# Optimization experiments

Hardware: AMD Instinct MI355X
Metric: run time of the kernel (lower is better)

Reference implementation:

```python
import jax, jax.numpy as jnp
import numpy as np

N_NODES = 50000
N_EDGES = 800000


def gcn_layer(x, edge_index, W, b):
    # GCNConv with normalize=False: out[i] = sum_{(j->i) in E} (x_j @ W) + b
    src, dst = edge_index[0], edge_index[1]
    h = x @ W                          # [N, F_out] transform first (cheaper)
    msg = h[src]                       # [E, F_out] gather
    agg = jax.ops.segment_sum(msg, dst, num_segments=x.shape[0])  # scatter-sum
    return agg + b


def setup_inputs() -> dict:
    key = jax.random.key(0)
    ks = jax.random.split(key, 6)
    x = jax.random.normal(ks[0], (N_NODES, 128), dtype=jnp.float32)
    edge_index = jax.random.randint(ks[1], (2, N_EDGES), 0, N_NODES, dtype=jnp.int64)
    # Glorot-ish scaling for stability through 3 layers
    W1 = jax.random.normal(ks[2], (128, 256), dtype=jnp.float32) * (1.0 / np.sqrt(128))
    W2 = jax.random.normal(ks[3], (256, 256), dtype=jnp.float32) * (1.0 / np.sqrt(256))
    W3 = jax.random.normal(ks[4], (256, 256), dtype=jnp.float32) * (1.0 / np.sqrt(256))
    b1 = jnp.zeros((256,), jnp.float32)
    b2 = jnp.zeros((256,), jnp.float32)
    b3 = jnp.zeros((256,), jnp.float32)
    return {"x": x, "edge_index": edge_index, "W1": W1, "b1": b1,
            "W2": W2, "b2": b2, "W3": W3, "b3": b3}


def reference(x, edge_index, W1, b1, W2, b2, W3, b3):
    h = jax.nn.relu(gcn_layer(x, edge_index, W1, b1))
    h = jax.nn.relu(gcn_layer(h, edge_index, W2, b2))
    h = jax.nn.relu(gcn_layer(h, edge_index, W3, b3))
    return h
```

## Files before the change

### kernel.cpp

```cpp
#include <hip/hip_runtime.h>
#include <hip/hip_bf16.h>


#define NBIN 98
#define BINSH 9

typedef short bf16x8 __attribute__((ext_vector_type(8)));
typedef float f32x4 __attribute__((ext_vector_type(4)));

__device__ __forceinline__ short f2bf(float f) {
    __hip_bfloat16 b = __float2bfloat16(f);
    return *reinterpret_cast<short*>(&b);
}
__device__ __forceinline__ float bf2f(short s) {
    union { unsigned u; float f; } c;
    c.u = ((unsigned)(unsigned short)s) << 16;
    return c.f;
}

__global__ void prep(const float* __restrict__ W1, const float* __restrict__ W2,
                     const float* __restrict__ W3, const float4* __restrict__ x,
                     short* __restrict__ Wt1, short* __restrict__ Wt2,
                     short* __restrict__ Wt3, short* __restrict__ xb) {
    int idx = blockIdx.x * 256 + threadIdx.x;
    if (idx < 32768) {
        int n = idx >> 7, k = idx & 127;
        Wt1[idx] = f2bf(W1[k * 256 + n]);
    } else if (idx < 98304) {
        int i = idx - 32768, n = i >> 8, k = i & 255;
        Wt2[i] = f2bf(W2[k * 256 + n]);
    } else if (idx < 163840) {
        int i = idx - 98304, n = i >> 8, k = i & 255;
        Wt3[i] = f2bf(W3[k * 256 + n]);
    } else {
        int i = idx - 163840;
        if (i < 1600000) {
            float4 v = x[i];
            short tmp[4] = { f2bf(v.x), f2bf(v.y), f2bf(v.z), f2bf(v.w) };
            *reinterpret_cast<uint2*>(&xb[i * 4]) = *reinterpret_cast<uint2*>(tmp);
        }
    }
}


__global__ void coarse_hist(const int* __restrict__ ei, int* __restrict__ cbin, int E) {
    __shared__ int h[NBIN];
    for (int i = threadIdx.x; i < NBIN; i += 256) h[i] = 0;
    __syncthreads();
    int base = blockIdx.x * 4096;
#pragma unroll
    for (int i = 0; i < 16; ++i) {
        int e = base + i * 256 + threadIdx.x;
        if (e < E) atomicAdd(&h[ei[E + e] >> BINSH], 1);
    }
    __syncthreads();
    for (int i = threadIdx.x; i < NBIN; i += 256)
        if (h[i]) atomicAdd(&cbin[i], h[i]);
}

__global__ void coarse_scan(const int* __restrict__ cbin, int* __restrict__ cstart,
                            int* __restrict__ gcursor, int* __restrict__ off,
                            int E, int N) {
    __shared__ int lds[128];
    int v = (threadIdx.x < NBIN) ? cbin[threadIdx.x] : 0;
    lds[threadIdx.x] = v;
    __syncthreads();
    for (int d = 1; d < 128; d <<= 1) {
        int t = (threadIdx.x >= d) ? lds[threadIdx.x - d] : 0;
        __syncthreads();
        lds[threadIdx.x] += t;
        __syncthreads();
    }
    if (threadIdx.x < NBIN) {
        int ex = lds[threadIdx.x] - v;
        cstart[threadIdx.x] = ex;
        gcursor[threadIdx.x] = ex;
    }
    if (threadIdx.x == 0) { cstart[NBIN] = E; off[N] = E; }
}

__global__ void bin_fill(const int* __restrict__ ei, int* __restrict__ gcursor,
                         unsigned* __restrict__ staging, int E) {
    __shared__ int h[NBIN];
    __shared__ int cur[NBIN];
    for (int i = threadIdx.x; i < NBIN; i += 256) h[i] = 0;
    __syncthreads();
    int base = blockIdx.x * 4096;
    int d_[16], s_[16];
#pragma unroll
    for (int i = 0; i < 16; ++i) {
        int e = base + i * 256 + threadIdx.x;
        if (e < E) {
            s_[i] = ei[e];
            d_[i] = ei[E + e];
            atomicAdd(&h[d_[i] >> BINSH], 1);
        } else d_[i] = -1;
    }
    __syncthreads();
    for (int i = threadIdx.x; i < NBIN; i += 256)
        cur[i] = h[i] ? atomicAdd(&gcursor[i], h[i]) : 0;
    __syncthreads();
#pragma unroll
    for (int i = 0; i < 16; ++i) {
        if (d_[i] >= 0) {
            int p = atomicAdd(&cur[d_[i] >> BINSH], 1);
            staging[p] = ((unsigned)(d_[i] & 511) << 16) | (unsigned)s_[i];
        }
    }
}

__global__ void bin_finalize(const unsigned* __restrict__ staging,
                             const int* __restrict__ cstart,
                             int* __restrict__ off, int* __restrict__ csr, int N) {
    __shared__ int cnt[512];
    __shared__ int psum[256];
    __shared__ int cur[512];
    const int b = blockIdx.x, t = threadIdx.x;
    cnt[t] = 0; cnt[t + 256] = 0;
    __syncthreads();
    const int s = cstart[b], e = cstart[b + 1];
    for (int p = s + t; p < e; p += 256) atomicAdd(&cnt[staging[p] >> 16], 1);
    __syncthreads();
    int c0 = cnt[2 * t], c1 = cnt[2 * t + 1];
    psum[t] = c0 + c1;
    __syncthreads();
    for (int d = 1; d < 256; d <<= 1) {
        int v = (t >= d) ? psum[t - d] : 0;
        __syncthreads();
        psum[t] += v;
        __syncthreads();
    }
    int base = s + (t ? psum[t - 1] : 0);
    int nb0 = b << BINSH;
    cur[2 * t] = base;
    cur[2 * t + 1] = base + c0;
    if (nb0 + 2 * t < N)     off[nb0 + 2 * t]     = base;
    if (nb0 + 2 * t + 1 < N) off[nb0 + 2 * t + 1] = base + c0;
    __syncthreads();
    for (int p = s + t; p < e; p += 256) {
        unsigned v = staging[p];
        int pos = atomicAdd(&cur[v >> 16], 1);
        csr[pos] = (int)(v & 0xFFFFu);
    }
}


template <int VEC>
__global__ void gather_csr_bf16(const short* __restrict__ h, short* __restrict__ agg,
                                const int* __restrict__ off, const int* __restrict__ csr,
                                int N) {
    typedef short svec __attribute__((ext_vector_type(VEC)));
    const int gw = (blockIdx.x * blockDim.x + threadIdx.x) >> 6;
    if (gw >= N) return;
    const int lane = threadIdx.x & 63;
    const int col = lane * VEC;
    const int F = 64 * VEC;
    const int base = off[gw];
    const int d = off[gw + 1] - base;

    float acc[VEC];
#pragma unroll
    for (int q = 0; q < VEC; ++q) acc[q] = 0.0f;

    int j = 0;
    for (; j + 4 <= d; j += 4) {
        int s0 = csr[base + j], s1 = csr[base + j + 1];
        int s2 = csr[base + j + 2], s3 = csr[base + j + 3];
        svec v0 = *reinterpret_cast<const svec*>(h + (size_t)s0 * F + col);
        svec v1 = *reinterpret_cast<const svec*>(h + (size_t)s1 * F + col);
        svec v2 = *reinterpret_cast<const svec*>(h + (size_t)s2 * F + col);
        svec v3 = *reinterpret_cast<const svec*>(h + (size_t)s3 * F + col);
#pragma unroll
        for (int q = 0; q < VEC; ++q)
            acc[q] += (bf2f(v0[q]) + bf2f(v1[q])) + (bf2f(v2[q]) + bf2f(v3[q]));
    }
    for (; j < d; ++j) {
        int s = csr[base + j];
        svec v = *reinterpret_cast<const svec*>(h + (size_t)s * F + col);
#pragma unroll
        for (int q = 0; q < VEC; ++q) acc[q] += bf2f(v[q]);
    }
    svec o;
#pragma unroll
    for (int q = 0; q < VEC; ++q) o[q] = f2bf(acc[q]);
    *reinterpret_cast<svec*>(agg + (size_t)gw * F + col) = o;
}


template <typename OutT>
__launch_bounds__(512)
__global__ void gemm_bias_relu(const short* __restrict__ A, const short* __restrict__ Wt,
                               const float* __restrict__ bias, OutT* __restrict__ out,
                               int M, int K) {
    __shared__ short As[128][72];
    __shared__ short Bs[256][72];

    const int tid = threadIdx.x;
    const int lane = tid & 63, wid = tid >> 6;
    const int wr = wid >> 2, wc = wid & 3;
    const int lr = lane & 15, lg = lane >> 4;
    const int m0 = blockIdx.x * 128;

    f32x4 acc[4][4];
#pragma unroll
    for (int i = 0; i < 4; ++i)
#pragma unroll
        for (int j = 0; j < 4; ++j)
#pragma unroll
            for (int r = 0; r < 4; ++r) acc[i][j][r] = 0.0f;

    const int srA = tid >> 2;
    const int scA = (tid & 3) << 4;
    const int srB = tid >> 1;
    const int scB = (tid & 1) << 5;

    for (int k0 = 0; k0 < K; k0 += 64) {
        __syncthreads();
        {
            int gm = m0 + srA;
            if (gm < M) {
                const uint4* ap = reinterpret_cast<const uint4*>(A + (size_t)gm * K + k0 + scA);
                *reinterpret_cast<uint4*>(&As[srA][scA])     = ap[0];
                *reinterpret_cast<uint4*>(&As[srA][scA + 8]) = ap[1];
            } else {
                uint4 z = {0, 0, 0, 0};
                *reinterpret_cast<uint4*>(&As[srA][scA])     = z;
                *reinterpret_cast<uint4*>(&As[srA][scA + 8]) = z;
            }
            const uint4* bp = reinterpret_cast<const uint4*>(Wt + (size_t)srB * K + k0 + scB);
            *reinterpret_cast<uint4*>(&Bs[srB][scB])      = bp[0];
            *reinterpret_cast<uint4*>(&Bs[srB][scB + 8])  = bp[1];
            *reinterpret_cast<uint4*>(&Bs[srB][scB + 16]) = bp[2];
            *reinterpret_cast<uint4*>(&Bs[srB][scB + 24]) = bp[3];
        }
        __syncthreads();

#pragma unroll
        for (int ksub = 0; ksub < 2; ++ksub) {
            const int kb = ksub * 32 + 4 * lg;
            bf16x8 a[4], b[4];
#pragma unroll
            for (int mi = 0; mi < 4; ++mi) {
                int row = wr * 64 + mi * 16 + lr;
                uint2* pa = reinterpret_cast<uint2*>(&a[mi]);
                pa[0] = *reinterpret_cast<const uint2*>(&As[row][kb]);
                pa[1] = *reinterpret_cast<const uint2*>(&As[row][kb + 16]);
            }
#pragma unroll
            for (int ni = 0; ni < 4; ++ni) {
                int row = wc * 64 + ni * 16 + lr;
                uint2* pb = reinterpret_cast<uint2*>(&b[ni]);
                pb[0] = *reinterpret_cast<const uint2*>(&Bs[row][kb]);
                pb[1] = *reinterpret_cast<const uint2*>(&Bs[row][kb + 16]);
            }
#pragma unroll
            for (int mi = 0; mi < 4; ++mi)
#pragma unroll
                for (int ni = 0; ni < 4; ++ni)
                    acc[mi][ni] = __builtin_amdgcn_mfma_f32_16x16x32_bf16(a[mi], b[ni], acc[mi][ni], 0, 0, 0);
        }
    }

    float bv[4];
#pragma unroll
    for (int ni = 0; ni < 4; ++ni) bv[ni] = bias[wc * 64 + ni * 16 + lr];
#pragma unroll
    for (int mi = 0; mi < 4; ++mi) {
        int gmBase = m0 + wr * 64 + mi * 16 + 4 * lg;
#pragma unroll
        for (int r = 0; r < 4; ++r) {
            int gm = gmBase + r;
            if (gm >= M) continue;
#pragma unroll
            for (int ni = 0; ni < 4; ++ni) {
                int gn = wc * 64 + ni * 16 + lr;
                float v = acc[mi][ni][r] + bv[ni];
                v = v > 0.0f ? v : 0.0f;
                if constexpr (sizeof(OutT) == 2)
                    out[(size_t)gm * 256 + gn] = (OutT)f2bf(v);
                else
                    out[(size_t)gm * 256 + gn] = (OutT)v;
            }
        }
    }
}

extern "C" void kernel_launch(void* const* d_in, const int* in_sizes, int n_in,
                              void* d_out, int out_size, void* d_ws, size_t ws_size,
                              hipStream_t stream) {
    const float* x  = (const float*)d_in[0];
    const int*   ei = (const int*)d_in[1];
    const float* W1 = (const float*)d_in[2];
    const float* b1 = (const float*)d_in[3];
    const float* W2 = (const float*)d_in[4];
    const float* b2 = (const float*)d_in[5];
    const float* W3 = (const float*)d_in[6];
    const float* b3 = (const float*)d_in[7];
    float* out = (float*)d_out;
    short* hb  = (short*)d_out;

    const int Nn = 50000, E = 800000, F0 = 128, F = 256;
    const int EB = (E + 4095) / 4096;

    short* aggb = (short*)d_ws;
    short* xb   = aggb + (size_t)Nn * F;
    short* Wt1  = xb + (size_t)Nn * F0;
    short* Wt2  = Wt1 + F0 * F;
    short* Wt3  = Wt2 + F * F;
    int* off     = (int*)(Wt3 + F * F);
    int* cbin    = off + Nn + 1;
    int* cstart  = cbin + NBIN;
    int* gcursor = cstart + NBIN + 1;
    unsigned* staging = (unsigned*)(gcursor + NBIN);
    int* csr     = (int*)(staging + E);

    prep<<<(163840 + 1600000 + 255) / 256, 256, 0, stream>>>(
        W1, W2, W3, (const float4*)x, Wt1, Wt2, Wt3, xb);

    hipMemsetAsync(cbin, 0, NBIN * 4, stream);
    coarse_hist<<<EB, 256, 0, stream>>>(ei, cbin, E);
    coarse_scan<<<1, 128, 0, stream>>>(cbin, cstart, gcursor, off, E, Nn);
    bin_fill<<<EB, 256, 0, stream>>>(ei, gcursor, staging, E);
    bin_finalize<<<NBIN, 256, 0, stream>>>(staging, cstart, off, csr, Nn);

    const int gemmGrid = (Nn + 127) / 128;
    const int gatherBlocks = (Nn * 64 + 255) / 256;

    gather_csr_bf16<2><<<gatherBlocks, 256, 0, stream>>>(xb, aggb, off, csr, Nn);
    gemm_bias_relu<short><<<gemmGrid, 512, 0, stream>>>(aggb, Wt1, b1, hb, Nn, F0);

    gather_csr_bf16<4><<<gatherBlocks, 256, 0, stream>>>(hb, aggb, off, csr, Nn);
    gemm_bias_relu<short><<<gemmGrid, 512, 0, stream>>>(aggb, Wt2, b2, hb, Nn, F);

    gather_csr_bf16<4><<<gatherBlocks, 256, 0, stream>>>(hb, aggb, off, csr, Nn);
    gemm_bias_relu<float><<<gemmGrid, 512, 0, stream>>>(aggb, Wt3, b3, out, Nn, F);
}
```

Measured before the change: 264.9 us.

## Drop coarse histogram pass via fixed-capacity bins; split-wave 16B gathers

CSR construction no longer runs a separate histogram kernel over the destinations. bin_fill writes into fixed-capacity per-bin staging regions (CAP slots each) and a small scan computes the bin bases afterwards. bin_finalize now sorts each bin by source bucket in LDS before scattering, which is meant to give more localized gather reads later. The gather kernels switch to 16-byte loads, with each wave handling several edges at once across half- or quarter-waves and combining results with shuffles. This risks overflow if any bin exceeds CAP entries, and it adds LDS pressure in finalize.

New measurement: 245.9 us. 7.2% less time.

```diff
diff --git a/kernel.cpp b/kernel.cpp
--- a/kernel.cpp
+++ b/kernel.cpp
@@ -4,6 +4,7 @@
 
 #define NBIN 98
 #define BINSH 9
+#define CAP 10240
 
 typedef short bf16x8 __attribute__((ext_vector_type(8)));
 typedef float f32x4 __attribute__((ext_vector_type(4)));
@@ -16,6 +17,18 @@
     union { unsigned u; float f; } c;
     c.u = ((unsigned)(unsigned short)s) << 16;
     return c.f;
+}
+
+__device__ __forceinline__ void acc8(float* a, uint4 v) {
+    unsigned w[4] = { v.x, v.y, v.z, v.w };
+#pragma unroll
+    for (int i = 0; i < 4; ++i) {
+        union { unsigned u; float f; } lo, hi;
+        lo.u = w[i] << 16;
+        hi.u = w[i] & 0xFFFF0000u;
+        a[2 * i]     += lo.f;
+        a[2 * i + 1] += hi.f;
+    }
 }
 
 __global__ void prep(const float* __restrict__ W1, const float* __restrict__ W2,
@@ -43,42 +56,6 @@
 }
 
 
-__global__ void coarse_hist(const int* __restrict__ ei, int* __restrict__ cbin, int E) {
-    __shared__ int h[NBIN];
-    for (int i = threadIdx.x; i < NBIN; i += 256) h[i] = 0;
-    __syncthreads();
-    int base = blockIdx.x * 4096;
-#pragma unroll
-    for (int i = 0; i < 16; ++i) {
-        int e = base + i * 256 + threadIdx.x;
-        if (e < E) atomicAdd(&h[ei[E + e] >> BINSH], 1);
-    }
-    __syncthreads();
-    for (int i = threadIdx.x; i < NBIN; i += 256)
-        if (h[i]) atomicAdd(&cbin[i], h[i]);
-}
-
-__global__ void coarse_scan(const int* __restrict__ cbin, int* __restrict__ cstart,
-                            int* __restrict__ gcursor, int* __restrict__ off,
-                            int E, int N) {
-    __shared__ int lds[128];
-    int v = (threadIdx.x < NBIN) ? cbin[threadIdx.x] : 0;
-    lds[threadIdx.x] = v;
-    __syncthreads();
-    for (int d = 1; d < 128; d <<= 1) {
-        int t = (threadIdx.x >= d) ? lds[threadIdx.x - d] : 0;
-        __syncthreads();
-        lds[threadIdx.x] += t;
-        __syncthreads();
-    }
-    if (threadIdx.x < NBIN) {
-        int ex = lds[threadIdx.x] - v;
-        cstart[threadIdx.x] = ex;
-        gcursor[threadIdx.x] = ex;
-    }
-    if (threadIdx.x == 0) { cstart[NBIN] = E; off[N] = E; }
-}
-
 __global__ void bin_fill(const int* __restrict__ ei, int* __restrict__ gcursor,
                          unsigned* __restrict__ staging, int E) {
     __shared__ int h[NBIN];
@@ -103,87 +80,186 @@
 #pragma unroll
     for (int i = 0; i < 16; ++i) {
         if (d_[i] >= 0) {
-            int p = atomicAdd(&cur[d_[i] >> BINSH], 1);
-            staging[p] = ((unsigned)(d_[i] & 511) << 16) | (unsigned)s_[i];
+            int bin = d_[i] >> BINSH;
+            int p = atomicAdd(&cur[bin], 1);
+            staging[(size_t)bin * CAP + p] =
+                ((unsigned)(d_[i] & 511) << 16) | (unsigned)s_[i];
         }
     }
 }
 
+__global__ void binbase_scan(const int* __restrict__ gcursor, int* __restrict__ binbase,
+                             int* __restrict__ off, int E, int N) {
+    __shared__ int lds[128];
+    int t = threadIdx.x;
+    int v = (t < NBIN) ? gcursor[t] : 0;
+    lds[t] = v;
+    __syncthreads();
+    for (int d = 1; d < 128; d <<= 1) {
+        int a = (t >= d) ? lds[t - d] : 0;
+        __syncthreads();
+        lds[t] += a;
+        __syncthreads();
+    }
+    if (t < NBIN) binbase[t] = lds[t] - v;
+    if (t == 0) off[N] = E;
+}
+
+__launch_bounds__(256)
 __global__ void bin_finalize(const unsigned* __restrict__ staging,
-                             const int* __restrict__ cstart,
+                             const int* __restrict__ cnt, const int* __restrict__ binbase,
                              int* __restrict__ off, int* __restrict__ csr, int N) {
-    __shared__ int cnt[512];
+    __shared__ unsigned sorted[CAP];
+    __shared__ int sb[128];
+    __shared__ int nd_c[512];
+    __shared__ int nd_pos[512];
     __shared__ int psum[256];
-    __shared__ int cur[512];
     const int b = blockIdx.x, t = threadIdx.x;
-    cnt[t] = 0; cnt[t + 256] = 0;
-    __syncthreads();
-    const int s = cstart[b], e = cstart[b + 1];
-    for (int p = s + t; p < e; p += 256) atomicAdd(&cnt[staging[p] >> 16], 1);
-    __syncthreads();
-    int c0 = cnt[2 * t], c1 = cnt[2 * t + 1];
+    const int n = cnt[b];
+    const unsigned* reg = staging + (size_t)b * CAP;
+    const int gbase = binbase[b];
+
+    if (t < 128) sb[t] = 0;
+    nd_c[t] = 0; nd_c[t + 256] = 0;
+    __syncthreads();
+    for (int p = t; p < n; p += 256) {
+        unsigned v = reg[p];
+        atomicAdd(&sb[(v & 0xFFFFu) >> BINSH], 1);
+        atomicAdd(&nd_c[v >> 16], 1);
+    }
+    __syncthreads();
+    int myc = (t < 128) ? sb[t] : 0;
+    for (int d = 1; d < 128; d <<= 1) {
+        int a = (t < 128 && t >= d) ? sb[t - d] : 0;
+        __syncthreads();
+        if (t < 128) sb[t] += a;
+        __syncthreads();
+    }
+    if (t < 128) sb[t] -= myc;
+    int c0 = nd_c[2 * t], c1 = nd_c[2 * t + 1];
     psum[t] = c0 + c1;
     __syncthreads();
     for (int d = 1; d < 256; d <<= 1) {
-        int v = (t >= d) ? psum[t - d] : 0;
-        __syncthreads();
-        psum[t] += v;
-        __syncthreads();
-    }
-    int base = s + (t ? psum[t - 1] : 0);
+        int a = (t >= d) ? psum[t - d] : 0;
+        __syncthreads();
+        psum[t] += a;
+        __syncthreads();
+    }
+    int ebase = gbase + (t ? psum[t - 1] : 0);
     int nb0 = b << BINSH;
-    cur[2 * t] = base;
-    cur[2 * t + 1] = base + c0;
-    if (nb0 + 2 * t < N)     off[nb0 + 2 * t]     = base;
-    if (nb0 + 2 * t + 1 < N) off[nb0 + 2 * t + 1] = base + c0;
-    __syncthreads();
-    for (int p = s + t; p < e; p += 256) {
-        unsigned v = staging[p];
-        int pos = atomicAdd(&cur[v >> 16], 1);
+    nd_pos[2 * t]     = ebase;
+    nd_pos[2 * t + 1] = ebase + c0;
+    if (nb0 + 2 * t < N)     off[nb0 + 2 * t]     = ebase;
+    if (nb0 + 2 * t + 1 < N) off[nb0 + 2 * t + 1] = ebase + c0;
+    __syncthreads();
+    for (int p = t; p < n; p += 256) {
+        unsigned v = reg[p];
+        int pos = atomicAdd(&sb[(v & 0xFFFFu) >> BINSH], 1);
+        sorted[pos] = v;
+    }
+    __syncthreads();
+    for (int p = t; p < n; p += 256) {
+        unsigned v = sorted[p];
+        int pos = atomicAdd(&nd_pos[v >> 16], 1);
         csr[pos] = (int)(v & 0xFFFFu);
     }
 }
 
 
-template <int VEC>
-__global__ void gather_csr_bf16(const short* __restrict__ h, short* __restrict__ agg,
-                                const int* __restrict__ off, const int* __restrict__ csr,
-                                int N) {
-    typedef short svec __attribute__((ext_vector_type(VEC)));
+__global__ void gather256(const short* __restrict__ h, short* __restrict__ agg,
+                          const int* __restrict__ off, const int* __restrict__ csr,
+                          int N) {
     const int gw = (blockIdx.x * blockDim.x + threadIdx.x) >> 6;
     if (gw >= N) return;
     const int lane = threadIdx.x & 63;
-    const int col = lane * VEC;
-    const int F = 64 * VEC;
+    const int half = lane >> 5, l = lane & 31;
+    const int col = l * 8;
     const int base = off[gw];
     const int d = off[gw + 1] - base;
 
-    float acc[VEC];
-#pragma unroll
-    for (int q = 0; q < VEC; ++q) acc[q] = 0.0f;
+    float acc[8];
+#pragma unroll
+    for (int q = 0; q < 8; ++q) acc[q] = 0.0f;
 
     int j = 0;
+    for (; j + 8 <= d; j += 8) {
+        int s0 = csr[base + j + half];
+        int s1 = csr[base + j + 2 + half];
+        int s2 = csr[base + j + 4 + half];
+        int s3 = csr[base + j + 6 + half];
+        uint4 v0 = *reinterpret_cast<const uint4*>(h + (size_t)s0 * 256 + col);
+        uint4 v1 = *reinterpret_cast<const uint4*>(h + (size_t)s1 * 256 + col);
+        uint4 v2 = *reinterpret_cast<const uint4*>(h + (size_t)s2 * 256 + col);
+        uint4 v3 = *reinterpret_cast<const uint4*>(h + (size_t)s3 * 256 + col);
+        acc8(acc, v0); acc8(acc, v1); acc8(acc, v2); acc8(acc, v3);
+    }
+    for (; j + 2 <= d; j += 2) {
+        int s = csr[base + j + half];
+        uint4 v = *reinterpret_cast<const uint4*>(h + (size_t)s * 256 + col);
+        acc8(acc, v);
+    }
+    if (j < d && half == 0) {
+        int s = csr[base + j];
+        uint4 v = *reinterpret_cast<const uint4*>(h + (size_t)s * 256 + col);
+        acc8(acc, v);
+    }
+#pragma unroll
+    for (int q = 0; q < 8; ++q) acc[q] += __shfl_xor(acc[q], 32);
+    if (half == 0) {
+        short o[8];
+#pragma unroll
+        for (int q = 0; q < 8; ++q) o[q] = f2bf(acc[q]);
+        *reinterpret_cast<uint4*>(agg + (size_t)gw * 256 + col) =
+            *reinterpret_cast<uint4*>(o);
+    }
+}
+
+__global__ void gather128(const short* __restrict__ h, short* __restrict__ agg,
+                          const int* __restrict__ off, const int* __restrict__ csr,
+                          int N) {
+    const int gw = (blockIdx.x * blockDim.x + threadIdx.x) >> 6;
+    if (gw >= N) return;
+    const int lane = threadIdx.x & 63;
+    const int q4 = lane >> 4, l = lane & 15;
+    const int col = l * 8;
+    const int base = off[gw];
+    const int d = off[gw + 1] - base;
+
+    float acc[8];
+#pragma unroll
+    for (int q = 0; q < 8; ++q) acc[q] = 0.0f;
+
+    int j = 0;
+    for (; j + 8 <= d; j += 8) {
+        int s0 = csr[base + j + q4];
+        int s1 = csr[base + j + 4 + q4];
+        uint4 v0 = *reinterpret_cast<const uint4*>(h + (size_t)s0 * 128 + col);
+        uint4 v1 = *reinterpret_cast<const uint4*>(h + (size_t)s1 * 128 + col);
+        acc8(acc, v0); acc8(acc, v1);
+    }
     for (; j + 4 <= d; j += 4) {
-        int s0 = csr[base + j], s1 = csr[base + j + 1];
-        int s2 = csr[base + j + 2], s3 = csr[base + j + 3];
-        svec v0 = *reinterpret_cast<const svec*>(h + (size_t)s0 * F + col);
-        svec v1 = *reinterpret_cast<const svec*>(h + (size_t)s1 * F + col);
-        svec v2 = *reinterpret_cast<const svec*>(h + (size_t)s2 * F + col);
-        svec v3 = *reinterpret_cast<const svec*>(h + (size_t)s3 * F + col);
-#pragma unroll
-        for (int q = 0; q < VEC; ++q)
-            acc[q] += (bf2f(v0[q]) + bf2f(v1[q])) + (bf2f(v2[q]) + bf2f(v3[q]));
-    }
-    for (; j < d; ++j) {
-        int s = csr[base + j];
-        svec v = *reinterpret_cast<const svec*>(h + (size_t)s * F + col);
-#pragma unroll
-        for (int q = 0; q < VEC; ++q) acc[q] += bf2f(v[q]);
-    }
-    svec o;
-#pragma unroll
-    for (int q = 0; q < VEC; ++q) o[q] = f2bf(acc[q]);
-    *reinterpret_cast<svec*>(agg + (size_t)gw * F + col) = o;
+        int s = csr[base + j + q4];
+        uint4 v = *reinterpret_cast<const uint4*>(h + (size_t)s * 128 + col);
+        acc8(acc, v);
+    }
+    int rem = d - j;
+    if (q4 < rem) {
+        int s = csr[base + j + q4];
+        uint4 v = *reinterpret_cast<const uint4*>(h + (size_t)s * 128 + col);
+        acc8(acc, v);
+    }
+#pragma unroll
+    for (int q = 0; q < 8; ++q) {
+        acc[q] += __shfl_xor(acc[q], 32);
+        acc[q] += __shfl_xor(acc[q], 16);
+    }
+    if (q4 == 0) {
+        short o[8];
+#pragma unroll
+        for (int q = 0; q < 8; ++q) o[q] = f2bf(acc[q]);
+        *reinterpret_cast<uint4*>(agg + (size_t)gw * 128 + col) =
+            *reinterpret_cast<uint4*>(o);
+    }
 }
 
 
@@ -308,30 +384,28 @@
     short* Wt2  = Wt1 + F0 * F;
     short* Wt3  = Wt2 + F * F;
     int* off     = (int*)(Wt3 + F * F);
-    int* cbin    = off + Nn + 1;
-    int* cstart  = cbin + NBIN;
-    int* gcursor = cstart + NBIN + 1;
-    unsigned* staging = (unsigned*)(gcursor + NBIN);
-    int* csr     = (int*)(staging + E);
+    int* gcursor = off + Nn + 1;
+    int* binbase = gcursor + NBIN;
+    unsigned* staging = (unsigned*)(binbase + NBIN);
+    int* csr     = (int*)(staging + (size_t)NBIN * CAP);
 
     prep<<<(163840 + 1600000 + 255) / 256, 256, 0, stream>>>(
         W1, W2, W3, (const float4*)x, Wt1, Wt2, Wt3, xb);
 
-    hipMemsetAsync(cbin, 0, NBIN * 4, stream);
-    coarse_hist<<<EB, 256, 0, stream>>>(ei, cbin, E);
-    coarse_scan<<<1, 128, 0, stream>>>(cbin, cstart, gcursor, off, E, Nn);
+    hipMemsetAsync(gcursor, 0, NBIN * 4, stream);
     bin_fill<<<EB, 256, 0, stream>>>(ei, gcursor, staging, E);
-    bin_finalize<<<NBIN, 256, 0, stream>>>(staging, cstart, off, csr, Nn);
+    binbase_scan<<<1, 128, 0, stream>>>(gcursor, binbase, off, E, Nn);
+    bin_finalize<<<NBIN, 256, 0, stream>>>(staging, gcursor, binbase, off, csr, Nn);
 
     const int gemmGrid = (Nn + 127) / 128;
     const int gatherBlocks = (Nn * 64 + 255) / 256;
 
-    gather_csr_bf16<2><<<gatherBlocks, 256, 0, stream>>>(xb, aggb, off, csr, Nn);
+    gather128<<<gatherBlocks, 256, 0, stream>>>(xb, aggb, off, csr, Nn);
     gemm_bias_relu<short><<<gemmGrid, 512, 0, stream>>>(aggb, Wt1, b1, hb, Nn, F0);
 
-    gather_csr_bf16<4><<<gatherBlocks, 256, 0, stream>>>(hb, aggb, off, csr, Nn);
+    gather256<<<gatherBlocks, 256, 0, stream>>>(hb, aggb, off, csr, Nn);
     gemm_bias_relu<short><<<gemmGrid, 512, 0, stream>>>(aggb, Wt2, b2, hb, Nn, F);
 
-    gather_csr_bf16<4><<<gatherBlocks, 256, 0, stream>>>(hb, aggb, off, csr, Nn);
+    gather256<<<gatherBlocks, 256, 0, stream>>>(hb, aggb, off, csr, Nn);
     gemm_bias_relu<float><<<gemmGrid, 512, 0, stream>>>(aggb, Wt3, b3, out, Nn, F);
 }
```
